# Kernel tuning notes

Hardware: AMD Instinct MI355X
Metric: run time of the kernel (lower is better)

Reference implementation:

```python
import jax, jax.numpy as jnp
import numpy as np

L, B, S, H = 2, 32, 2048, 512  # layers, batch, src_len, hidden_size
D = 2 * H                      # feature dim of hidden / encoder_outputs


def setup_inputs() -> dict:
    key = jax.random.key(0)
    k1, k2, k3, k4, k5 = jax.random.split(key, 5)
    scale = 1.0 / np.sqrt(4 * H)
    return {
        "hidden": jax.random.normal(k1, (L, B, D), dtype=jnp.float32),
        "encoder_outputs": jax.random.normal(k2, (B, S, D), dtype=jnp.float32),
        "attn_w": jax.random.normal(k3, (H, 4 * H), dtype=jnp.float32) * scale,
        "attn_b": jax.random.normal(k4, (H,), dtype=jnp.float32) * scale,
        "v_w": jax.random.normal(k5, (1, H), dtype=jnp.float32) * (1.0 / np.sqrt(H)),
    }


def reference(hidden, encoder_outputs, attn_w, attn_b, v_w):
    # hidden: [L, B, D]; permute(1,0,2) then [:, -1, :] == last layer state [B, D]
    h = hidden[-1]  # [B, D]
    # Avoid materializing the [B,S,2D] concat: split attn_w into the block acting
    # on the (repeated) hidden part and the block acting on encoder_outputs.
    w_h, w_e = attn_w[:, :D], attn_w[:, D:]          # [H, D] each
    # hidden contribution is constant over src_len -> compute once per batch row
    e_h = jnp.einsum('bd,hd->bh', h, w_h)            # [B, H]
    e_e = jnp.einsum('bsd,hd->bsh', encoder_outputs, w_e)  # [B, S, H]
    energy = jnp.tanh(e_e + e_h[:, None, :] + attn_b)      # [B, S, H]
    scores = jnp.einsum('bsh,h->bs', energy, v_w[0])       # [B, S]
    attention_weights = jax.nn.softmax(scores, axis=1)     # [B, S]
    context = jnp.einsum('bs,bsd->bd', attention_weights, encoder_outputs)
    return (context[:, None, :], attention_weights[:, None, :])
```

## Files before the change

kernel.cpp:

```cpp
#include <hip/hip_runtime.h>
#include <math.h>

#define LL 2
#define BB 32
#define SS 2048
#define HH 512
#define DD 1024
#define W4S 2048

#define BM 64
#define BN 256
#define BK 64
#define NT (DD / BK)
#define ASTR 72

typedef __attribute__((ext_vector_type(8))) short bf16x8;
typedef __attribute__((ext_vector_type(4))) float f32x4;

__device__ inline unsigned pk2_rne(float a, float b) {
    unsigned ua = __float_as_uint(a), ub = __float_as_uint(b);
    unsigned ra = (ua + 0x7fffu + ((ua >> 16) & 1u)) >> 16;
    unsigned rb = (ub + 0x7fffu + ((ub >> 16) & 1u)) & 0xffff0000u;
    return ra | rb;
}

__device__ inline unsigned pk2_hu(float a, float b) {
    unsigned ua = __float_as_uint(a) + 0x8000u;
    unsigned ub = __float_as_uint(b) + 0x8000u;
    return __builtin_amdgcn_perm(ub, ua, 0x07060302u);
}

__device__ inline float fast_tanh(float x) {
    x = fminf(9.f, fmaxf(-9.f, x));
    float e = __expf(2.f * x);
    return 1.f - 2.f * __builtin_amdgcn_rcpf(e + 1.f);
}

__device__ inline void gl_lds16(const unsigned short* g, short* l) {
    __builtin_amdgcn_global_load_lds(
        (const __attribute__((address_space(1))) unsigned int*)g,
        (__attribute__((address_space(3))) unsigned int*)l, 16, 0, 0);
}

__global__ void k_zero(float* __restrict__ scores) {
    scores[blockIdx.x * 256 + threadIdx.x] = 0.f;
}

__global__ __launch_bounds__(256) void k_pack(const float* __restrict__ attn_w,
                                              unsigned short* __restrict__ Bp) {
    int h = blockIdx.x, t = threadIdx.x;
    float4 v = *(const float4*)(attn_w + (size_t)h * W4S + DD + t * 4);
    uint2 r = make_uint2(pk2_rne(v.x, v.y), pk2_rne(v.z, v.w));
    *(uint2*)(Bp + (size_t)h * DD + t * 4) = r;
}

__global__ __launch_bounds__(256) void k_base(const float* __restrict__ hidden,
                                              const float* __restrict__ attn_w,
                                              const float* __restrict__ attn_b,
                                              float* __restrict__ base) {
    int wid  = (blockIdx.x * 256 + threadIdx.x) >> 6;
    int lane = threadIdx.x & 63;
    int b = wid >> 9;
    int h = wid & (HH - 1);
    const float4* h4 = (const float4*)(hidden + (size_t)(LL - 1) * BB * DD + (size_t)b * DD);
    const float4* w4 = (const float4*)(attn_w + (size_t)h * W4S);
    float s = 0.f;
    #pragma unroll
    for (int i = 0; i < 4; i++) {
        float4 a = h4[lane + i * 64], w = w4[lane + i * 64];
        s += a.x * w.x + a.y * w.y + a.z * w.z + a.w * w.w;
    }
    #pragma unroll
    for (int off = 32; off; off >>= 1) s += __shfl_xor(s, off);
    if (lane == 0) base[b * HH + h] = s + attn_b[h];
}

__global__ __launch_bounds__(256, 2) void k_scores(const float* __restrict__ enc,
                                                   const unsigned short* __restrict__ Bp,
                                                   const float* __restrict__ base,
                                                   const float* __restrict__ vw,
                                                   float* __restrict__ scores) {
    __shared__ short As[BM * ASTR];
    __shared__ short Bs[2][BN * BK];

    const int tid  = threadIdx.x;
    const int wid  = tid >> 6;
    const int lane = tid & 63;
    const int lm   = lane & 15;
    const int kq   = lane >> 4;
    const int n0   = blockIdx.x * BN;
    const int m0   = blockIdx.y * BM;
    const int b    = m0 >> 11;
    const int wn   = wid * 64;

    const int rowA = tid >> 3;
    const int gA   = tid & 7;
    const float* Ag0 = enc + (size_t)(m0 + rowA) * DD + gA * 8;
    const float* Ag1 = Ag0 + (size_t)32 * DD;
    short* AsW0 = As + rowA * ASTR + gA * 8;
    short* AsW1 = AsW0 + 32 * ASTR;

    const int brow = lane >> 3;
    const int bgsw = (lane & 7) ^ brow;
    const unsigned short* Bg = Bp + (size_t)(n0 + wn + brow) * DD + bgsw * 8;

    f32x4 acc[4][4];
    #pragma unroll
    for (int i = 0; i < 4; i++)
        #pragma unroll
        for (int j = 0; j < 4; j++) acc[i][j] = (f32x4){0.f, 0.f, 0.f, 0.f};

    #pragma unroll
    for (int i = 0; i < 8; i++)
        gl_lds16(Bg + (size_t)(i * 8) * DD, &Bs[0][(wn + i * 8) * BK]);
    float4 a0 = *(const float4*)(Ag0);
    float4 a1 = *(const float4*)(Ag0 + 4);
    float4 a2 = *(const float4*)(Ag1);
    float4 a3 = *(const float4*)(Ag1 + 4);

    for (int kt = 0; kt < NT; kt++) {
        __syncthreads();
        uint4 p0 = {pk2_hu(a0.x, a0.y), pk2_hu(a0.z, a0.w),
                    pk2_hu(a1.x, a1.y), pk2_hu(a1.z, a1.w)};
        uint4 p1 = {pk2_hu(a2.x, a2.y), pk2_hu(a2.z, a2.w),
                    pk2_hu(a3.x, a3.y), pk2_hu(a3.z, a3.w)};
        *(uint4*)AsW0 = p0;
        *(uint4*)AsW1 = p1;
        __syncthreads();
        if (kt + 1 < NT) {
            #pragma unroll
            for (int i = 0; i < 8; i++)
                gl_lds16(Bg + (size_t)(i * 8) * DD + (kt + 1) * BK,
                         &Bs[(kt + 1) & 1][(wn + i * 8) * BK]);
            a0 = *(const float4*)(Ag0 + (kt + 1) * BK);
            a1 = *(const float4*)(Ag0 + (kt + 1) * BK + 4);
            a2 = *(const float4*)(Ag1 + (kt + 1) * BK);
            a3 = *(const float4*)(Ag1 + (kt + 1) * BK + 4);
        }
        const short* Bb = Bs[kt & 1];
        #pragma unroll
        for (int s = 0; s < 2; s++) {
            bf16x8 af[4];
            #pragma unroll
            for (int mi = 0; mi < 4; mi++)
                af[mi] = *(const bf16x8*)&As[(mi * 16 + lm) * ASTR + (s * 4 + kq) * 8];
            #pragma unroll
            for (int ni = 0; ni < 4; ni++) {
                bf16x8 bf = *(const bf16x8*)
                    &Bb[(wn + ni * 16 + lm) * BK + (((s * 4 + kq)) ^ (lm & 7)) * 8];
                #pragma unroll
                for (int mi = 0; mi < 4; mi++)
                    acc[mi][ni] = __builtin_amdgcn_mfma_f32_16x16x32_bf16(
                        af[mi], bf, acc[mi][ni], 0, 0, 0);
            }
        }
    }

    const float* basep = base + b * HH + n0 + wn;
    const float* vp    = vw + n0 + wn;
    float p[4][4] = {};
    #pragma unroll
    for (int ni = 0; ni < 4; ni++) {
        int nl = ni * 16 + lm;
        float bs = basep[nl];
        float vv = vp[nl];
        #pragma unroll
        for (int mi = 0; mi < 4; mi++)
            #pragma unroll
            for (int r = 0; r < 4; r++)
                p[mi][r] += vv * fast_tanh(acc[mi][ni][r] + bs);
    }
    #pragma unroll
    for (int off = 8; off; off >>= 1)
        #pragma unroll
        for (int mi = 0; mi < 4; mi++)
            #pragma unroll
            for (int r = 0; r < 4; r++)
                p[mi][r] += __shfl_xor(p[mi][r], off);
    if (lm == 0) {
        #pragma unroll
        for (int mi = 0; mi < 4; mi++)
            #pragma unroll
            for (int r = 0; r < 4; r++)
                atomicAdd(&scores[m0 + mi * 16 + kq * 4 + r], p[mi][r]);
    }
}

__global__ __launch_bounds__(256) void k_softmax(const float* __restrict__ scores,
                                                 float* __restrict__ wout) {
    int b = blockIdx.x, tid = threadIdx.x;
    const float* rowp = scores + b * SS;
    float v[8];
    float m = -1e30f;
    #pragma unroll
    for (int i = 0; i < 8; i++) { v[i] = rowp[tid + i * 256]; m = fmaxf(m, v[i]); }
    __shared__ float sm[4], ssum[4];
    #pragma unroll
    for (int off = 32; off; off >>= 1) m = fmaxf(m, __shfl_xor(m, off));
    if ((tid & 63) == 0) sm[tid >> 6] = m;
    __syncthreads();
    m = fmaxf(fmaxf(sm[0], sm[1]), fmaxf(sm[2], sm[3]));
    float s = 0.f;
    #pragma unroll
    for (int i = 0; i < 8; i++) { v[i] = __expf(v[i] - m); s += v[i]; }
    #pragma unroll
    for (int off = 32; off; off >>= 1) s += __shfl_xor(s, off);
    if ((tid & 63) == 0) ssum[tid >> 6] = s;
    __syncthreads();
    s = ssum[0] + ssum[1] + ssum[2] + ssum[3];
    float inv = 1.f / s;
    #pragma unroll
    for (int i = 0; i < 8; i++) wout[b * SS + tid + i * 256] = v[i] * inv;
}

#define CCH 64
__global__ __launch_bounds__(256) void k_ctxpart(const float* __restrict__ enc,
                                                 const float* __restrict__ w,
                                                 float* __restrict__ part) {
    int b = blockIdx.x, c = blockIdx.y, tid = threadIdx.x;
    __shared__ float wsh[CCH];
    if (tid < CCH) wsh[tid] = w[b * SS + c * CCH + tid];
    __syncthreads();
    const float4* e4 = (const float4*)(enc + ((size_t)b * SS + c * CCH) * DD);
    float4 acc = {0.f, 0.f, 0.f, 0.f};
    #pragma unroll 8
    for (int s = 0; s < CCH; s++) {
        float wv  = wsh[s];
        float4 ev = e4[(size_t)s * (DD / 4) + tid];
        acc.x += wv * ev.x; acc.y += wv * ev.y;
        acc.z += wv * ev.z; acc.w += wv * ev.w;
    }
    *(float4*)(part + (size_t)(b * 32 + c) * DD + tid * 4) = acc;
}

__global__ __launch_bounds__(256) void k_ctxreduce(const float* __restrict__ part,
                                                   float* __restrict__ ctx) {
    int b = blockIdx.x, d = blockIdx.y * 256 + threadIdx.x;
    float s = 0.f;
    #pragma unroll
    for (int c = 0; c < 32; c++) s += part[(size_t)(b * 32 + c) * DD + d];
    ctx[b * DD + d] = s;
}

extern "C" void kernel_launch(void* const* d_in, const int* in_sizes, int n_in,
                              void* d_out, int out_size, void* d_ws, size_t ws_size,
                              hipStream_t stream) {
    const float* hidden = (const float*)d_in[0];
    const float* enc    = (const float*)d_in[1];
    const float* attn_w = (const float*)d_in[2];
    const float* attn_b = (const float*)d_in[3];
    const float* v_w    = (const float*)d_in[4];

    float* out      = (float*)d_out;
    float* ctx_out  = out;
    float* attn_out = out + BB * DD;

    float* base   = (float*)d_ws;
    float* scores = base + BB * HH;
    unsigned short* Bp = (unsigned short*)(scores + BB * SS);
    float* part   = (float*)(Bp + (size_t)HH * DD);

    hipLaunchKernelGGL(k_zero, dim3(BB * SS / 256), dim3(256), 0, stream, scores);
    hipLaunchKernelGGL(k_pack, dim3(HH), dim3(256), 0, stream, attn_w, Bp);
    hipLaunchKernelGGL(k_base, dim3(BB * HH / 4), dim3(256), 0, stream,
                       hidden, attn_w, attn_b, base);
    hipLaunchKernelGGL(k_scores, dim3(2, BB * SS / BM), dim3(256), 0, stream,
                       enc, Bp, base, v_w, scores);
    hipLaunchKernelGGL(k_softmax, dim3(BB), dim3(256), 0, stream, scores, attn_out);
    hipLaunchKernelGGL(k_ctxpart, dim3(BB, SS / CCH), dim3(256), 0, stream,
                       enc, attn_out, part);
    hipLaunchKernelGGL(k_ctxreduce, dim3(BB, DD / 256), dim3(256), 0, stream,
                       part, ctx_out);
}
```

Measured before the change: 478.7 us.

## Fragment-major LDS layout, double-buffer A, merge prep kernels, fuse softmax normalize

Rewrites the scores GEMM so A and B tiles are stored in LDS in MFMA fragment order, so each lane reads its fragment contiguously, and double-buffers the bf16 A tile with two-step-ahead register prefetch so one barrier per k-step is removed. Each wave now loads its own 16 rows of A and its 64 columns of B. The zero, pack and base kernels are merged into one launch. Softmax is split into a stats kernel plus normalization fused into the context partial kernel, which also writes the attention weights. This trades more register pressure for fewer barriers, fewer launches and one less pass over the scores.

```diff
diff --git a/kernel.cpp b/kernel.cpp
--- a/kernel.cpp
+++ b/kernel.cpp
@@ -12,7 +12,6 @@
 #define BN 256
 #define BK 64
 #define NT (DD / BK)
-#define ASTR 72
 
 typedef __attribute__((ext_vector_type(8))) short bf16x8;
 typedef __attribute__((ext_vector_type(4))) float f32x4;
@@ -42,23 +41,27 @@
         (__attribute__((address_space(3))) unsigned int*)l, 16, 0, 0);
 }
 
-__global__ void k_zero(float* __restrict__ scores) {
-    scores[blockIdx.x * 256 + threadIdx.x] = 0.f;
-}
-
-__global__ __launch_bounds__(256) void k_pack(const float* __restrict__ attn_w,
-                                              unsigned short* __restrict__ Bp) {
-    int h = blockIdx.x, t = threadIdx.x;
-    float4 v = *(const float4*)(attn_w + (size_t)h * W4S + DD + t * 4);
-    uint2 r = make_uint2(pk2_rne(v.x, v.y), pk2_rne(v.z, v.w));
-    *(uint2*)(Bp + (size_t)h * DD + t * 4) = r;
-}
-
-__global__ __launch_bounds__(256) void k_base(const float* __restrict__ hidden,
+__global__ __launch_bounds__(256) void k_prep(const float* __restrict__ hidden,
                                               const float* __restrict__ attn_w,
                                               const float* __restrict__ attn_b,
-                                              float* __restrict__ base) {
-    int wid  = (blockIdx.x * 256 + threadIdx.x) >> 6;
+                                              unsigned short* __restrict__ Bp,
+                                              float* __restrict__ base,
+                                              float* __restrict__ scores) {
+    int bx = blockIdx.x;
+    if (bx < BB * SS / 256) {
+        scores[bx * 256 + threadIdx.x] = 0.f;
+        return;
+    }
+    bx -= BB * SS / 256;
+    if (bx < HH) {
+        int t = threadIdx.x;
+        float4 v = *(const float4*)(attn_w + (size_t)bx * W4S + DD + t * 4);
+        *(uint2*)(Bp + (size_t)bx * DD + t * 4) =
+            make_uint2(pk2_rne(v.x, v.y), pk2_rne(v.z, v.w));
+        return;
+    }
+    bx -= HH;
+    int wid  = bx * 4 + (threadIdx.x >> 6);
     int lane = threadIdx.x & 63;
     int b = wid >> 9;
     int h = wid & (HH - 1);
@@ -80,8 +83,8 @@
                                                    const float* __restrict__ base,
                                                    const float* __restrict__ vw,
                                                    float* __restrict__ scores) {
-    __shared__ short As[BM * ASTR];
-    __shared__ short Bs[2][BN * BK];
+    __shared__ short As[2][8 * 64 * 8];
+    __shared__ short Bs[2][4][8 * 64 * 8];
 
     const int tid  = threadIdx.x;
     const int wid  = tid >> 6;
@@ -91,18 +94,33 @@
     const int n0   = blockIdx.x * BN;
     const int m0   = blockIdx.y * BM;
     const int b    = m0 >> 11;
-    const int wn   = wid * 64;
-
-    const int rowA = tid >> 3;
-    const int gA   = tid & 7;
-    const float* Ag0 = enc + (size_t)(m0 + rowA) * DD + gA * 8;
-    const float* Ag1 = Ag0 + (size_t)32 * DD;
-    short* AsW0 = As + rowA * ASTR + gA * 8;
-    short* AsW1 = AsW0 + 32 * ASTR;
-
-    const int brow = lane >> 3;
-    const int bgsw = (lane & 7) ^ brow;
-    const unsigned short* Bg = Bp + (size_t)(n0 + wn + brow) * DD + bgsw * 8;
+    const int wn   = n0 + wid * 64;
+
+    const float* Ag = enc + (size_t)(m0 + wid * 16 + lm) * DD + kq * 8;
+    const unsigned short* Bgl = Bp + (size_t)(wn + lm) * DD + kq * 8;
+
+    #pragma unroll
+    for (int ni = 0; ni < 4; ni++)
+        #pragma unroll
+        for (int s = 0; s < 2; s++)
+            gl_lds16(Bgl + (size_t)ni * 16 * DD + s * 32,
+                     &Bs[0][wid][(ni * 2 + s) * 64 * 8]);
+
+    float4 ra[2][4];
+    #pragma unroll
+    for (int s = 0; s < 2; s++) {
+        ra[0][s * 2 + 0] = *(const float4*)(Ag + s * 32);
+        ra[0][s * 2 + 1] = *(const float4*)(Ag + s * 32 + 4);
+        ra[1][s * 2 + 0] = *(const float4*)(Ag + 64 + s * 32);
+        ra[1][s * 2 + 1] = *(const float4*)(Ag + 64 + s * 32 + 4);
+    }
+    #pragma unroll
+    for (int s = 0; s < 2; s++) {
+        float4 x = ra[0][s * 2], y = ra[0][s * 2 + 1];
+        uint4 p = {pk2_hu(x.x, x.y), pk2_hu(x.z, x.w),
+                   pk2_hu(y.x, y.y), pk2_hu(y.z, y.w)};
+        *(uint4*)&As[0][((wid * 2 + s) * 64 + lane) * 8] = p;
+    }
 
     f32x4 acc[4][4];
     #pragma unroll
@@ -110,44 +128,41 @@
         #pragma unroll
         for (int j = 0; j < 4; j++) acc[i][j] = (f32x4){0.f, 0.f, 0.f, 0.f};
 
-    #pragma unroll
-    for (int i = 0; i < 8; i++)
-        gl_lds16(Bg + (size_t)(i * 8) * DD, &Bs[0][(wn + i * 8) * BK]);
-    float4 a0 = *(const float4*)(Ag0);
-    float4 a1 = *(const float4*)(Ag0 + 4);
-    float4 a2 = *(const float4*)(Ag1);
-    float4 a3 = *(const float4*)(Ag1 + 4);
-
+    #pragma unroll 2
     for (int kt = 0; kt < NT; kt++) {
-        __syncthreads();
-        uint4 p0 = {pk2_hu(a0.x, a0.y), pk2_hu(a0.z, a0.w),
-                    pk2_hu(a1.x, a1.y), pk2_hu(a1.z, a1.w)};
-        uint4 p1 = {pk2_hu(a2.x, a2.y), pk2_hu(a2.z, a2.w),
-                    pk2_hu(a3.x, a3.y), pk2_hu(a3.z, a3.w)};
-        *(uint4*)AsW0 = p0;
-        *(uint4*)AsW1 = p1;
+        const int c = kt & 1;
         __syncthreads();
         if (kt + 1 < NT) {
             #pragma unroll
-            for (int i = 0; i < 8; i++)
-                gl_lds16(Bg + (size_t)(i * 8) * DD + (kt + 1) * BK,
-                         &Bs[(kt + 1) & 1][(wn + i * 8) * BK]);
-            a0 = *(const float4*)(Ag0 + (kt + 1) * BK);
-            a1 = *(const float4*)(Ag0 + (kt + 1) * BK + 4);
-            a2 = *(const float4*)(Ag1 + (kt + 1) * BK);
-            a3 = *(const float4*)(Ag1 + (kt + 1) * BK + 4);
+            for (int ni = 0; ni < 4; ni++)
+                #pragma unroll
+                for (int s = 0; s < 2; s++)
+                    gl_lds16(Bgl + (size_t)ni * 16 * DD + (kt + 1) * 64 + s * 32,
+                             &Bs[c ^ 1][wid][(ni * 2 + s) * 64 * 8]);
+            if (kt + 2 < NT) {
+                #pragma unroll
+                for (int s = 0; s < 2; s++) {
+                    ra[c][s * 2 + 0] = *(const float4*)(Ag + (kt + 2) * 64 + s * 32);
+                    ra[c][s * 2 + 1] = *(const float4*)(Ag + (kt + 2) * 64 + s * 32 + 4);
+                }
+            }
+            #pragma unroll
+            for (int s = 0; s < 2; s++) {
+                float4 x = ra[c ^ 1][s * 2], y = ra[c ^ 1][s * 2 + 1];
+                uint4 p = {pk2_hu(x.x, x.y), pk2_hu(x.z, x.w),
+                           pk2_hu(y.x, y.y), pk2_hu(y.z, y.w)};
+                *(uint4*)&As[c ^ 1][((wid * 2 + s) * 64 + lane) * 8] = p;
+            }
         }
-        const short* Bb = Bs[kt & 1];
         #pragma unroll
         for (int s = 0; s < 2; s++) {
             bf16x8 af[4];
             #pragma unroll
             for (int mi = 0; mi < 4; mi++)
-                af[mi] = *(const bf16x8*)&As[(mi * 16 + lm) * ASTR + (s * 4 + kq) * 8];
+                af[mi] = *(const bf16x8*)&As[c][((mi * 2 + s) * 64 + lane) * 8];
             #pragma unroll
             for (int ni = 0; ni < 4; ni++) {
-                bf16x8 bf = *(const bf16x8*)
-                    &Bb[(wn + ni * 16 + lm) * BK + (((s * 4 + kq)) ^ (lm & 7)) * 8];
+                bf16x8 bf = *(const bf16x8*)&Bs[c][wid][((ni * 2 + s) * 64 + lane) * 8];
                 #pragma unroll
                 for (int mi = 0; mi < 4; mi++)
                     acc[mi][ni] = __builtin_amdgcn_mfma_f32_16x16x32_bf16(
@@ -156,8 +171,8 @@
         }
     }
 
-    const float* basep = base + b * HH + n0 + wn;
-    const float* vp    = vw + n0 + wn;
+    const float* basep = base + b * HH + wn;
+    const float* vp    = vw + wn;
     float p[4][4] = {};
     #pragma unroll
     for (int ni = 0; ni < 4; ni++) {
@@ -186,8 +201,8 @@
     }
 }
 
-__global__ __launch_bounds__(256) void k_softmax(const float* __restrict__ scores,
-                                                 float* __restrict__ wout) {
+__global__ __launch_bounds__(256) void k_smstat(const float* __restrict__ scores,
+                                                float2* __restrict__ stat) {
     int b = blockIdx.x, tid = threadIdx.x;
     const float* rowp = scores + b * SS;
     float v[8];
@@ -202,24 +217,31 @@
     m = fmaxf(fmaxf(sm[0], sm[1]), fmaxf(sm[2], sm[3]));
     float s = 0.f;
     #pragma unroll
-    for (int i = 0; i < 8; i++) { v[i] = __expf(v[i] - m); s += v[i]; }
+    for (int i = 0; i < 8; i++) s += __expf(v[i] - m);
     #pragma unroll
     for (int off = 32; off; off >>= 1) s += __shfl_xor(s, off);
     if ((tid & 63) == 0) ssum[tid >> 6] = s;
     __syncthreads();
-    s = ssum[0] + ssum[1] + ssum[2] + ssum[3];
-    float inv = 1.f / s;
-    #pragma unroll
-    for (int i = 0; i < 8; i++) wout[b * SS + tid + i * 256] = v[i] * inv;
+    if (tid == 0) {
+        float tot = ssum[0] + ssum[1] + ssum[2] + ssum[3];
+        stat[b] = make_float2(m, 1.f / tot);
+    }
 }
 
 #define CCH 64
 __global__ __launch_bounds__(256) void k_ctxpart(const float* __restrict__ enc,
-                                                 const float* __restrict__ w,
+                                                 const float* __restrict__ scores,
+                                                 const float2* __restrict__ stat,
+                                                 float* __restrict__ attn_out,
                                                  float* __restrict__ part) {
     int b = blockIdx.x, c = blockIdx.y, tid = threadIdx.x;
     __shared__ float wsh[CCH];
-    if (tid < CCH) wsh[tid] = w[b * SS + c * CCH + tid];
+    float2 st = stat[b];
+    if (tid < CCH) {
+        float w = __expf(scores[b * SS + c * CCH + tid] - st.x) * st.y;
+        wsh[tid] = w;
+        attn_out[b * SS + c * CCH + tid] = w;
+    }
     __syncthreads();
     const float4* e4 = (const float4*)(enc + ((size_t)b * SS + c * CCH) * DD);
     float4 acc = {0.f, 0.f, 0.f, 0.f};
@@ -255,20 +277,19 @@
     float* ctx_out  = out;
     float* attn_out = out + BB * DD;
 
-    float* base   = (float*)d_ws;
-    float* scores = base + BB * HH;
+    float* base        = (float*)d_ws;
+    float* scores      = base + BB * HH;
     unsigned short* Bp = (unsigned short*)(scores + BB * SS);
-    float* part   = (float*)(Bp + (size_t)HH * DD);
-
-    hipLaunchKernelGGL(k_zero, dim3(BB * SS / 256), dim3(256), 0, stream, scores);
-    hipLaunchKernelGGL(k_pack, dim3(HH), dim3(256), 0, stream, attn_w, Bp);
-    hipLaunchKernelGGL(k_base, dim3(BB * HH / 4), dim3(256), 0, stream,
-                       hidden, attn_w, attn_b, base);
+    float2* stat       = (float2*)(Bp + (size_t)HH * DD);
+    float* part        = (float*)(stat + BB);
+
+    hipLaunchKernelGGL(k_prep, dim3(BB * SS / 256 + HH + BB * HH / 4), dim3(256),
+                       0, stream, hidden, attn_w, attn_b, Bp, base, scores);
     hipLaunchKernelGGL(k_scores, dim3(2, BB * SS / BM), dim3(256), 0, stream,
                        enc, Bp, base, v_w, scores);
-    hipLaunchKernelGGL(k_softmax, dim3(BB), dim3(256), 0, stream, scores, attn_out);
+    hipLaunchKernelGGL(k_smstat, dim3(BB), dim3(256), 0, stream, scores, stat);
     hipLaunchKernelGGL(k_ctxpart, dim3(BB, SS / CCH), dim3(256), 0, stream,
-                       enc, attn_out, part);
+                       enc, scores, stat, attn_out, part);
     hipLaunchKernelGGL(k_ctxreduce, dim3(BB, DD / 256), dim3(256), 0, stream,
                        part, ctx_out);
 }
```

After: 521.6 us. +8.9%, slower.
